# Optimization experiments

Hardware: AMD Instinct MI355X
Metric: run time of the kernel (lower is better)

The kernel has to match this reference:

```python
import jax, jax.numpy as jnp
import numpy as np

N_HEADS = 16


def setup_inputs() -> dict:
    key = jax.random.key(0)
    ks = jax.random.split(key, 5)
    B, S, D = 2, 2048, 1024
    x = jax.random.normal(ks[0], (B, S, D), dtype=jnp.float32)
    Wqkv = jax.random.normal(ks[1], (D, 3 * D), dtype=jnp.float32) * (1.0 / np.sqrt(D))
    bqkv = jax.random.normal(ks[2], (3 * D,), dtype=jnp.float32) * 0.02
    Wout = jax.random.normal(ks[3], (D, D), dtype=jnp.float32) * (1.0 / np.sqrt(D))
    bout = jax.random.normal(ks[4], (D,), dtype=jnp.float32) * 0.02
    return {"x": x, "Wqkv": Wqkv, "bqkv": bqkv, "Wout": Wout, "bout": bout}


def reference(x, Wqkv, bqkv, Wout, bout):
    B, S, D = x.shape
    H = N_HEADS
    dh = D // H
    # qkv projection, then view as [B,S,H,3*dh] and chunk on last dim
    # (matches torch: per-head q/k/v are interleaved slices of the projection)
    qkv = (x @ Wqkv + bqkv).reshape(B, S, H, 3 * dh).transpose(0, 2, 1, 3)  # [B,H,S,3dh]
    q, k, v = jnp.split(qkv, 3, axis=-1)  # each [B,H,S,dh]
    scale = jnp.asarray(1.0 / np.sqrt(dh), dtype=x.dtype)
    scores = jnp.einsum('bhqd,bhkd->bhqk', q, k) * scale  # [B,H,S,S]
    causal = jnp.tril(jnp.ones((S, S), dtype=bool))
    scores = jnp.where(causal, scores, jnp.asarray(-jnp.inf, dtype=scores.dtype))
    attn_w = jax.nn.softmax(scores, axis=-1)
    attn = jnp.einsum('bhqk,bhkd->bhqd', attn_w, v)  # [B,H,S,dh]
    attn = attn.transpose(0, 2, 1, 3).reshape(B, S, D)
    return attn @ Wout + bout
```

## Files before the change

### kernel.cpp

```cpp
#include <hip/hip_runtime.h>
#include <hip/hip_bf16.h>
#include <cstdint>
#include <cstddef>

typedef __hip_bfloat16 bf16;
typedef short bf16x4 __attribute__((ext_vector_type(4)));
typedef short bf16x8 __attribute__((ext_vector_type(8)));
typedef float f32x4 __attribute__((ext_vector_type(4)));

#define LOG2E 1.44269504088896f

static constexpr int Bb = 2, S = 2048, D = 1024, H = 16, DH = 64;

__device__ inline short f2bf_bits(float f) {
  bf16 b = __float2bfloat16(f);
  short s;
  __builtin_memcpy(&s, &b, 2);
  return s;
}

__global__ void transpose_cvt_k(const float* __restrict__ in, bf16* __restrict__ out,
                                int R, int C) {
  __shared__ float t[32][33];
  int c0 = blockIdx.x * 32, r0 = blockIdx.y * 32;
  int tx = threadIdx.x, ty = threadIdx.y;
#pragma unroll
  for (int i = 0; i < 4; i++) {
    int r = ty + i * 8;
    t[r][tx] = in[(size_t)(r0 + r) * C + c0 + tx];
  }
  __syncthreads();
#pragma unroll
  for (int i = 0; i < 4; i++) {
    int c = ty + i * 8;
    out[(size_t)(c0 + c) * R + r0 + tx] = __float2bfloat16(t[tx][c]);
  }
}

__global__ void cvt_f32_bf16_k(const float* __restrict__ in, bf16* __restrict__ out) {
  size_t i = ((size_t)blockIdx.x * 256 + threadIdx.x) * 8;
  f32x4 a = *(const f32x4*)(in + i);
  f32x4 b = *(const f32x4*)(in + i + 4);
  bf16x8 v;
#pragma unroll
  for (int j = 0; j < 4; j++) { v[j] = f2bf_bits(a[j]); v[4 + j] = f2bf_bits(b[j]); }
  *(bf16x8*)((short*)out + i) = v;
}

__global__ __launch_bounds__(256) void gemm_qkv(
    const bf16* __restrict__ A, const bf16* __restrict__ Bt,
    const float* __restrict__ bias,
    bf16* __restrict__ Qb, bf16* __restrict__ Kb, bf16* __restrict__ Vtb) {
  constexpr int K = 1024, N = 3072;
  __shared__ __align__(16) short smA[128 * 32];
  __shared__ __align__(16) short smB[128 * 32];

  const int tid = threadIdx.x;
  const int wave = tid >> 6, lane = tid & 63;
  const int quad = lane >> 4, l16 = lane & 15;
  const int m0 = blockIdx.y * 128, n0 = blockIdx.x * 128;
  const int wm = wave >> 1, wn = wave & 1;

  f32x4 acc[4][4];
#pragma unroll
  for (int i = 0; i < 4; i++)
#pragma unroll
    for (int j = 0; j < 4; j++) acc[i][j] = {0.f, 0.f, 0.f, 0.f};

  const int srow = lane >> 2;
  const int scol = (lane & 3) * 8;

  for (int k0 = 0; k0 < K; k0 += 32) {
#pragma unroll
    for (int half = 0; half < 2; half++) {
      int row = half * 64 + wave * 16 + srow;
      const bf16* ga = A + (size_t)(m0 + row) * K + k0 + scol;
      const bf16* gb = Bt + (size_t)(n0 + row) * K + k0 + scol;
      __builtin_amdgcn_global_load_lds(
          (const __attribute__((address_space(1))) void*)ga,
          (__attribute__((address_space(3))) void*)&smA[(half * 64 + wave * 16) * 32],
          16, 0, 0);
      __builtin_amdgcn_global_load_lds(
          (const __attribute__((address_space(1))) void*)gb,
          (__attribute__((address_space(3))) void*)&smB[(half * 64 + wave * 16) * 32],
          16, 0, 0);
    }
    __syncthreads();

    bf16x8 af[4], bf_[4];
#pragma unroll
    for (int mi = 0; mi < 4; mi++)
      af[mi] = *(const bf16x8*)&smA[(wm * 64 + mi * 16 + l16) * 32 + quad * 8];
#pragma unroll
    for (int ni = 0; ni < 4; ni++)
      bf_[ni] = *(const bf16x8*)&smB[(wn * 64 + ni * 16 + l16) * 32 + quad * 8];
#pragma unroll
    for (int mi = 0; mi < 4; mi++)
#pragma unroll
      for (int ni = 0; ni < 4; ni++)
        acc[mi][ni] = __builtin_amdgcn_mfma_f32_16x16x32_bf16(
            af[mi], bf_[ni], acc[mi][ni], 0, 0, 0);
    __syncthreads();
  }

#pragma unroll
  for (int ni = 0; ni < 4; ni++) {
    const int cs = n0 + wn * 64 + ni * 16;
    const int h = cs / 192;
    const int roff = cs - h * 192;
    const float bv = bias[cs + l16];
#pragma unroll
    for (int mi = 0; mi < 4; mi++) {
      const int t0 = m0 + wm * 64 + mi * 16 + quad * 4;
      const int b = t0 >> 11, s0 = t0 & 2047;
      if (roff < 64) {
        const int dh = roff + l16;
        size_t base = ((size_t)(b * H + h) * S + s0) * 64 + dh;
#pragma unroll
        for (int r = 0; r < 4; r++)
          Qb[base + (size_t)r * 64] = __float2bfloat16(acc[mi][ni][r] + bv);
      } else if (roff < 128) {
        const int dh = roff - 64 + l16;
        size_t base = ((size_t)(b * H + h) * S + s0) * 64 + dh;
#pragma unroll
        for (int r = 0; r < 4; r++)
          Kb[base + (size_t)r * 64] = __float2bfloat16(acc[mi][ni][r] + bv);
      } else {
        const int dh = roff - 128 + l16;
        size_t base = ((size_t)(b * H + h) * 64 + dh) * S + s0;
        bf16x4 vv;
#pragma unroll
        for (int r = 0; r < 4; r++) vv[r] = f2bf_bits(acc[mi][ni][r] + bv);
        *(bf16x4*)((short*)Vtb + base) = vv;
      }
    }
  }
}

template <typename TC, int BN>
__global__ __launch_bounds__(256) void gemm_bt_bias(
    const bf16* __restrict__ A, const bf16* __restrict__ Bt,
    const float* __restrict__ bias, TC* __restrict__ C,
    int M, int N, int K) {
  constexpr int NF = BN / 32;
  __shared__ __align__(16) short smA[128 * 32];
  __shared__ __align__(16) short smB[BN * 32];

  const int tid = threadIdx.x;
  const int wave = tid >> 6, lane = tid & 63;
  const int quad = lane >> 4, l16 = lane & 15;
  const int m0 = blockIdx.y * 128, n0 = blockIdx.x * BN;
  const int wm = wave >> 1, wn = wave & 1;

  f32x4 acc[4][NF];
#pragma unroll
  for (int i = 0; i < 4; i++)
#pragma unroll
    for (int j = 0; j < NF; j++) acc[i][j] = {0.f, 0.f, 0.f, 0.f};

  const int srow = lane >> 2;
  const int scol = (lane & 3) * 8;

  for (int k0 = 0; k0 < K; k0 += 32) {
#pragma unroll
    for (int half = 0; half < 2; half++) {
      int row = half * 64 + wave * 16 + srow;
      const bf16* ga = A + (size_t)(m0 + row) * K + k0 + scol;
      __builtin_amdgcn_global_load_lds(
          (const __attribute__((address_space(1))) void*)ga,
          (__attribute__((address_space(3))) void*)&smA[(half * 64 + wave * 16) * 32],
          16, 0, 0);
    }
#pragma unroll
    for (int half = 0; half < BN / 64; half++) {
      int row = half * 64 + wave * 16 + srow;
      const bf16* gb = Bt + (size_t)(n0 + row) * K + k0 + scol;
      __builtin_amdgcn_global_load_lds(
          (const __attribute__((address_space(1))) void*)gb,
          (__attribute__((address_space(3))) void*)&smB[(half * 64 + wave * 16) * 32],
          16, 0, 0);
    }
    __syncthreads();

    bf16x8 af[4], bf_[NF];
#pragma unroll
    for (int mi = 0; mi < 4; mi++)
      af[mi] = *(const bf16x8*)&smA[(wm * 64 + mi * 16 + l16) * 32 + quad * 8];
#pragma unroll
    for (int ni = 0; ni < NF; ni++)
      bf_[ni] = *(const bf16x8*)&smB[(wn * (BN / 2) + ni * 16 + l16) * 32 + quad * 8];
#pragma unroll
    for (int mi = 0; mi < 4; mi++)
#pragma unroll
      for (int ni = 0; ni < NF; ni++)
        acc[mi][ni] = __builtin_amdgcn_mfma_f32_16x16x32_bf16(
            af[mi], bf_[ni], acc[mi][ni], 0, 0, 0);
    __syncthreads();
  }

#pragma unroll
  for (int ni = 0; ni < NF; ni++) {
    int col = n0 + wn * (BN / 2) + ni * 16 + l16;
    float bv = bias[col];
#pragma unroll
    for (int mi = 0; mi < 4; mi++) {
#pragma unroll
      for (int r = 0; r < 4; r++) {
        int row = m0 + wm * 64 + mi * 16 + quad * 4 + r;
        float v = acc[mi][ni][r] + bv;
        if constexpr (__is_same(TC, float))
          C[(size_t)row * N + col] = v;
        else
          C[(size_t)row * N + col] = __float2bfloat16(v);
      }
    }
  }
}

__global__ __launch_bounds__(256) void attn_kernel(
    const bf16* __restrict__ Qb, const bf16* __restrict__ Kb,
    const bf16* __restrict__ Vtb, bf16* __restrict__ O) {
  const int p = blockIdx.x & 15, bh = blockIdx.x >> 4;
  const int h = bh & (H - 1), b = bh >> 4;
  const int tid = threadIdx.x;
  const int wave = tid >> 6, lane = tid & 63;
  const int quad = lane >> 4, l16 = lane & 15;

  const bf16* Qh = Qb + (size_t)(b * H + h) * S * 64;
  const bf16* Kh = Kb + (size_t)(b * H + h) * S * 64;
  const bf16* Vth = Vtb + (size_t)(b * H + h) * 64 * S;

  __shared__ __align__(16) short smK[64 * 64];
  __shared__ __align__(16) short smVt[64 * 64];
  __shared__ __align__(16) short pLds[4][16][72];

  const int lrow = lane >> 3;
  const int lg = lane & 7;

  const float PSCALE = 0.125f * LOG2E;
  const int swz = l16 & 7;

#pragma unroll
  for (int pass = 0; pass < 2; pass++) {
    const int qt = pass ? p : (31 - p);
    const int q0 = qt * 64 + wave * 16;

    bf16x8 aQ[2];
#pragma unroll
    for (int kh = 0; kh < 2; kh++)
      aQ[kh] = *(const bf16x8*)(Qh + (size_t)(q0 + l16) * 64 + kh * 32 + quad * 8);

    f32x4 o[4];
#pragma unroll
    for (int dt = 0; dt < 4; dt++) o[dt] = {0.f, 0.f, 0.f, 0.f};
    float lsum[4] = {0.f, 0.f, 0.f, 0.f};

    const int ntiles = qt + 1;
    for (int it = 0; it < ntiles; it++) {
      const int kv0 = it * 64;
      __syncthreads();

#pragma unroll
      for (int j = 0; j < 2; j++) {
        const int row = wave * 16 + j * 8 + lrow;
        const bf16* ks = Kh + (size_t)(kv0 + row) * 64 + (lg ^ (row & 7)) * 8;
        __builtin_amdgcn_global_load_lds(
            (const __attribute__((address_space(1))) void*)ks,
            (__attribute__((address_space(3))) void*)&smK[(wave * 16 + j * 8) * 64],
            16, 0, 0);
        const bf16* vs = Vth + (size_t)row * S + kv0 + (lg ^ (row & 7)) * 8;
        __builtin_amdgcn_global_load_lds(
            (const __attribute__((address_space(1))) void*)vs,
            (__attribute__((address_space(3))) void*)&smVt[(wave * 16 + j * 8) * 64],
            16, 0, 0);
      }
      __syncthreads();

      f32x4 z[4];
#pragma unroll
      for (int nh = 0; nh < 4; nh++) {
        const int row = nh * 16 + l16;
        f32x4 t = {0.f, 0.f, 0.f, 0.f};
#pragma unroll
        for (int kh = 0; kh < 2; kh++) {
          bf16x8 bK = *(const bf16x8*)&smK[row * 64 + ((kh * 4 + quad) ^ swz) * 8];
          t = __builtin_amdgcn_mfma_f32_16x16x32_bf16(aQ[kh], bK, t, 0, 0, 0);
        }
        z[nh] = t;
      }

      const bool full = (it < qt);

#pragma unroll
      for (int r = 0; r < 4; r++) {
        const int qrow = wave * 16 + quad * 4 + r;
        float pv[4];
#pragma unroll
        for (int nh = 0; nh < 4; nh++) {
          float e = exp2f(z[nh][r] * PSCALE);
          pv[nh] = (full || (nh * 16 + l16 <= qrow)) ? e : 0.f;
        }
        lsum[r] += (pv[0] + pv[1]) + (pv[2] + pv[3]);
#pragma unroll
        for (int nh = 0; nh < 4; nh++)
          pLds[wave][quad * 4 + r][nh * 16 + l16] = f2bf_bits(pv[nh]);
      }

      asm volatile("s_waitcnt lgkmcnt(0)" ::: "memory");

      bf16x8 aP[2];
#pragma unroll
      for (int k2 = 0; k2 < 2; k2++)
        aP[k2] = *(const bf16x8*)&pLds[wave][l16][k2 * 32 + quad * 8];
#pragma unroll
      for (int dt = 0; dt < 4; dt++) {
        const int row = dt * 16 + l16;
#pragma unroll
        for (int k2 = 0; k2 < 2; k2++) {
          bf16x8 bV = *(const bf16x8*)&smVt[row * 64 + ((k2 * 4 + quad) ^ swz) * 8];
          o[dt] = __builtin_amdgcn_mfma_f32_16x16x32_bf16(aP[k2], bV, o[dt], 0, 0, 0);
        }
      }
    }

#pragma unroll
    for (int r = 0; r < 4; r++) {
      float l = lsum[r];
#pragma unroll
      for (int d = 1; d < 16; d <<= 1) l += __shfl_xor(l, d, 64);
      const float inv = 1.f / l;
      const int q = q0 + quad * 4 + r;
#pragma unroll
      for (int dt = 0; dt < 4; dt++)
        O[(size_t)(b * S + q) * D + h * 64 + dt * 16 + l16] =
            __float2bfloat16(o[dt][r] * inv);
    }
  }
}

extern "C" void kernel_launch(void* const* d_in, const int* in_sizes, int n_in,
                              void* d_out, int out_size, void* d_ws, size_t ws_size,
                              hipStream_t stream) {
  const float* x    = (const float*)d_in[0];
  const float* Wqkv = (const float*)d_in[1];
  const float* bqkv = (const float*)d_in[2];
  const float* Wout = (const float*)d_in[3];
  const float* bout = (const float*)d_in[4];
  float* out = (float*)d_out;

  char* ws = (char*)d_ws;
  bf16* Qb    = (bf16*)(ws);
  bf16* Kb    = (bf16*)(ws + 8388608);
  bf16* Vtb   = (bf16*)(ws + 16777216);
  bf16* xbf   = (bf16*)(ws + 25165824);
  bf16* attnO = (bf16*)(ws + 25165824);
  bf16* wqkvT = (bf16*)(ws + 33554432);
  bf16* woutT = (bf16*)(ws + 39845888);

  transpose_cvt_k<<<dim3(3072 / 32, 1024 / 32), dim3(32, 8), 0, stream>>>(Wqkv, wqkvT, 1024, 3072);
  transpose_cvt_k<<<dim3(1024 / 32, 1024 / 32), dim3(32, 8), 0, stream>>>(Wout, woutT, 1024, 1024);
  cvt_f32_bf16_k<<<dim3(4096 * 1024 / (256 * 8)), 256, 0, stream>>>(x, xbf);

  gemm_qkv<<<dim3(3072 / 128, 4096 / 128), 256, 0, stream>>>(
      xbf, wqkvT, bqkv, Qb, Kb, Vtb);

  attn_kernel<<<dim3(Bb * H * (S / 128)), 256, 0, stream>>>(Qb, Kb, Vtb, attnO);

  gemm_bt_bias<float, 64><<<dim3(1024 / 64, 4096 / 128), 256, 0, stream>>>(
      attnO, woutT, bout, out, 4096, 1024, 1024);
}
```

Before: 200.9 us.

## Split causal attention KV loop across two blocks and add reduce kernel

The attention kernel can now run in a split-KV mode. Two blocks per query tile process alternating KV tiles and write unnormalized partial outputs plus row sums to workspace, and a new reduce kernel adds them, normalizes and writes the head-interleaved layout. This doubles the grid from 512 to 1024 blocks to improve CU occupancy and load balance. The cost is an extra launch, extra global traffic for the partials, and bf16 rounding of partial sums. The split path only runs when the workspace is large enough. The P staging buffer row padding is also changed from 72 to 76.

New measurement: 197.8 us. About the same (-1.6%).

```diff
diff --git a/kernel.cpp b/kernel.cpp
--- a/kernel.cpp
+++ b/kernel.cpp
@@ -18,6 +18,12 @@
   __builtin_memcpy(&s, &b, 2);
   return s;
 }
+__device__ inline float bfbits2f(short s) {
+  uint32_t u = ((uint32_t)(uint16_t)s) << 16;
+  float f;
+  __builtin_memcpy(&f, &u, 4);
+  return f;
+}
 
 __global__ void transpose_cvt_k(const float* __restrict__ in, bf16* __restrict__ out,
                                 int R, int C) {
@@ -51,7 +57,7 @@
     const bf16* __restrict__ A, const bf16* __restrict__ Bt,
     const float* __restrict__ bias,
     bf16* __restrict__ Qb, bf16* __restrict__ Kb, bf16* __restrict__ Vtb) {
-  constexpr int K = 1024, N = 3072;
+  constexpr int K = 1024;
   __shared__ __align__(16) short smA[128 * 32];
   __shared__ __align__(16) short smB[128 * 32];
 
@@ -219,24 +225,32 @@
 
 __global__ __launch_bounds__(256) void attn_kernel(
     const bf16* __restrict__ Qb, const bf16* __restrict__ Kb,
-    const bf16* __restrict__ Vtb, bf16* __restrict__ O) {
-  const int p = blockIdx.x & 15, bh = blockIdx.x >> 4;
+    const bf16* __restrict__ Vtb,
+    bf16* __restrict__ Op0, bf16* __restrict__ Op1,
+    float* __restrict__ lp0, float* __restrict__ lp1,
+    bf16* __restrict__ Ofinal, int split) {
+  const int blk = blockIdx.x;
+  int sk, p, bh;
+  if (split == 2) { sk = blk & 1; p = (blk >> 1) & 15; bh = blk >> 5; }
+  else            { sk = 0;       p = blk & 15;        bh = blk >> 4; }
   const int h = bh & (H - 1), b = bh >> 4;
   const int tid = threadIdx.x;
   const int wave = tid >> 6, lane = tid & 63;
   const int quad = lane >> 4, l16 = lane & 15;
 
+  bf16* __restrict__ Op = sk ? Op1 : Op0;
+  float* __restrict__ lp = sk ? lp1 : lp0;
+
   const bf16* Qh = Qb + (size_t)(b * H + h) * S * 64;
   const bf16* Kh = Kb + (size_t)(b * H + h) * S * 64;
   const bf16* Vth = Vtb + (size_t)(b * H + h) * 64 * S;
 
   __shared__ __align__(16) short smK[64 * 64];
   __shared__ __align__(16) short smVt[64 * 64];
-  __shared__ __align__(16) short pLds[4][16][72];
+  __shared__ __align__(16) short pLds[4][16][76];
 
   const int lrow = lane >> 3;
   const int lg = lane & 7;
-
   const float PSCALE = 0.125f * LOG2E;
   const int swz = l16 & 7;
 
@@ -255,8 +269,7 @@
     for (int dt = 0; dt < 4; dt++) o[dt] = {0.f, 0.f, 0.f, 0.f};
     float lsum[4] = {0.f, 0.f, 0.f, 0.f};
 
-    const int ntiles = qt + 1;
-    for (int it = 0; it < ntiles; it++) {
+    for (int it = sk; it <= qt; it += split) {
       const int kv0 = it * 64;
       __syncthreads();
 
@@ -328,14 +341,41 @@
       float l = lsum[r];
 #pragma unroll
       for (int d = 1; d < 16; d <<= 1) l += __shfl_xor(l, d, 64);
-      const float inv = 1.f / l;
       const int q = q0 + quad * 4 + r;
-#pragma unroll
-      for (int dt = 0; dt < 4; dt++)
-        O[(size_t)(b * S + q) * D + h * 64 + dt * 16 + l16] =
-            __float2bfloat16(o[dt][r] * inv);
-    }
-  }
+      const size_t row = (size_t)(b * H + h) * S + q;
+      if (split == 2) {
+        if (l16 == 0) lp[row] = l;
+#pragma unroll
+        for (int dt = 0; dt < 4; dt++)
+          ((short*)Op)[row * 64 + dt * 16 + l16] = f2bf_bits(o[dt][r]);
+      } else {
+        const float inv = 1.f / l;
+#pragma unroll
+        for (int dt = 0; dt < 4; dt++)
+          Ofinal[(size_t)(b * S + q) * D + h * 64 + dt * 16 + l16] =
+              __float2bfloat16(o[dt][r] * inv);
+      }
+    }
+  }
+}
+
+__global__ __launch_bounds__(256) void attn_reduce(
+    const bf16* __restrict__ O0, const bf16* __restrict__ O1,
+    const float* __restrict__ l0, const float* __restrict__ l1,
+    bf16* __restrict__ attnO) {
+  int gid = blockIdx.x * 256 + threadIdx.x;
+  int row = gid >> 3;
+  int c8 = (gid & 7) * 8;
+  float inv = 1.f / (l0[row] + l1[row]);
+  bf16x8 a = *(const bf16x8*)((const short*)O0 + (size_t)row * 64 + c8);
+  bf16x8 bb = *(const bf16x8*)((const short*)O1 + (size_t)row * 64 + c8);
+  bf16x8 o;
+#pragma unroll
+  for (int j = 0; j < 8; j++)
+    o[j] = f2bf_bits((bfbits2f(a[j]) + bfbits2f(bb[j])) * inv);
+  int bh = row >> 11, q = row & 2047;
+  int b = bh >> 4, h = bh & 15;
+  *(bf16x8*)((short*)attnO + (((size_t)(b * S + q) * H + h) * 64 + c8)) = o;
 }
 
 extern "C" void kernel_launch(void* const* d_in, const int* in_sizes, int n_in,
@@ -349,13 +389,30 @@
   float* out = (float*)d_out;
 
   char* ws = (char*)d_ws;
-  bf16* Qb    = (bf16*)(ws);
-  bf16* Kb    = (bf16*)(ws + 8388608);
-  bf16* Vtb   = (bf16*)(ws + 16777216);
-  bf16* xbf   = (bf16*)(ws + 25165824);
-  bf16* attnO = (bf16*)(ws + 25165824);
-  bf16* wqkvT = (bf16*)(ws + 33554432);
-  bf16* woutT = (bf16*)(ws + 39845888);
+  const bool split2 = (ws_size >= 50855936);
+
+  bf16* Qb  = (bf16*)(ws);
+  bf16* Kb  = (bf16*)(ws + 8388608);
+  bf16* Vtb = (bf16*)(ws + 16777216);
+  bf16* xbf = (bf16*)(ws + 25165824);
+
+  bf16 *Op0, *Op1, *attnO;
+  float *lp0, *lp1;
+  bf16 *wqkvT, *woutT;
+  if (split2) {
+    Op0   = (bf16*)(ws + 25165824);
+    Op1   = (bf16*)(ws + 33554432);
+    lp0   = (float*)(ws + 41943040);
+    lp1   = (float*)(ws + 42205184);
+    attnO = (bf16*)(ws + 8388608);
+    wqkvT = (bf16*)(ws + 42467328);
+    woutT = (bf16*)(ws + 48758784);
+  } else {
+    Op0 = Op1 = nullptr; lp0 = lp1 = nullptr;
+    attnO = (bf16*)(ws + 25165824);
+    wqkvT = (bf16*)(ws + 33554432);
+    woutT = (bf16*)(ws + 39845888);
+  }
 
   transpose_cvt_k<<<dim3(3072 / 32, 1024 / 32), dim3(32, 8), 0, stream>>>(Wqkv, wqkvT, 1024, 3072);
   transpose_cvt_k<<<dim3(1024 / 32, 1024 / 32), dim3(32, 8), 0, stream>>>(Wout, woutT, 1024, 1024);
@@ -364,7 +421,14 @@
   gemm_qkv<<<dim3(3072 / 128, 4096 / 128), 256, 0, stream>>>(
       xbf, wqkvT, bqkv, Qb, Kb, Vtb);
 
-  attn_kernel<<<dim3(Bb * H * (S / 128)), 256, 0, stream>>>(Qb, Kb, Vtb, attnO);
+  if (split2) {
+    attn_kernel<<<dim3(1024), 256, 0, stream>>>(
+        Qb, Kb, Vtb, Op0, Op1, lp0, lp1, nullptr, 2);
+    attn_reduce<<<dim3(2048), 256, 0, stream>>>(Op0, Op1, lp0, lp1, attnO);
+  } else {
+    attn_kernel<<<dim3(512), 256, 0, stream>>>(
+        Qb, Kb, Vtb, nullptr, nullptr, nullptr, nullptr, attnO, 1);
+  }
 
   gemm_bt_bias<float, 64><<<dim3(1024 / 64, 4096 / 128), 256, 0, stream>>>(
       attnO, woutT, bout, out, 4096, 1024, 1024);
```
